# Optimization experiments

Hardware: AMD Instinct MI355X
Metric: run time of the kernel (lower is better)

The kernel has to match this reference:

```python
import jax, jax.numpy as jnp
import numpy as np
from jax.scipy.linalg import solve_triangular

JITTER = 1e-5
BIG = 1e9


def _rq(d2, outscale, ls, alpha):
    # Rational-quadratic kernel (gpytorch RQKernel with outputscale)
    return outscale * (1.0 + d2 / (2.0 * alpha * ls * ls)) ** (-alpha)


def _per_var(tb, m, nz, os_, ls, al, K):
    # tb: [L] times of one sample; m: [L] bool, points belonging to this variable.
    # Sequential GP fantasy updates == prefix conditioning. chol of a leading
    # principal block equals leading block of full chol, so one Cholesky +
    # one triangular solve + cumsum over rows reproduces the sequential loop.
    L = tb.shape[0]
    keyt = jnp.where(m, tb, BIG)
    order = jnp.argsort(keyt)            # this variable's points, time-sorted, first
    ts = tb[order]
    ms = m[order]
    mf = ms.astype(tb.dtype)
    d2 = (ts[:, None] - ts[None, :]) ** 2
    Kxx = _rq(d2, os_, ls, al) * (mf[:, None] * mf[None, :])  # masked rows/cols -> 0
    idx = jnp.arange(L)
    # noisy train covariance; masked points get identity rows (decoupled, zero effect)
    Kn = Kxx.at[idx, idx].set(jnp.where(ms, os_ + nz + JITTER, 1.0))
    C = jnp.linalg.cholesky(Kn)
    v = solve_triangular(C, Kxx, lower=True)     # [L train, L test] (test = same points)
    cum = jnp.cumsum(v * v, axis=0)              # variance explained after i obs
    std_pref = jnp.sqrt(jnp.maximum(os_ - cum, 1e-12)) * mf[None, :]
    sums = std_pref.sum(axis=1)                  # sum of posterior stds after each obs
    s0 = jnp.sqrt(os_) * mf.sum()                # prior sum of stds
    prev = jnp.concatenate([s0[None], sums[:-1]])
    gains = jnp.maximum(prev - sums, 0.0) * mf   # info gain per added observation
    # partition timeline into K groups of near-equal total information
    cg = jnp.cumsum(gains)
    frac = (cg - 0.5 * gains) / jnp.maximum(cg[-1], 1e-12)
    grp = jnp.clip(jnp.floor(frac * K), 0, K - 1).astype(jnp.int32)
    return order, mf, grp, gains


def _forward(t, vid, noise, outputscale, lengthscale, alpha, K):
    B, L = t.shape
    V = noise.shape[0]

    def per_bv(tb, vidb, v):
        m = vidb == v
        order, mf, grp, gains = _per_var(tb, m, noise[v], outputscale[v],
                                         lengthscale[v], alpha[v], K)
        col = v * K + grp
        oh = jnp.zeros((L, V * K), t.dtype).at[order, col].add(mf)
        g = jnp.zeros((L,), t.dtype).at[order].add(gains)
        return oh, g

    def per_b(tb, vidb):
        oh, g = jax.vmap(per_bv, in_axes=(None, None, 0))(tb, vidb, jnp.arange(V))
        return oh.sum(0), g.sum(0)   # variables are disjoint -> sum == union

    return jax.vmap(per_b)(t, vid)


def setup_inputs() -> dict:
    key = jax.random.key(0)
    ks = jax.random.split(key, 7)
    B, L, V = 8, 512, 16
    t = jax.random.uniform(ks[0], (B, L), dtype=jnp.float32)
    y = jax.random.normal(ks[1], (B, L), dtype=jnp.float32)
    vid = jax.random.randint(ks[2], (B, L), 0, V, dtype=jnp.int32)
    noise = 0.01 + 0.05 * jax.random.uniform(ks[3], (V,), dtype=jnp.float32)
    outputscale = 0.5 + jax.random.uniform(ks[4], (V,), dtype=jnp.float32)
    lengthscale = 0.05 + 0.2 * jax.random.uniform(ks[5], (V,), dtype=jnp.float32)
    alpha = 0.5 + jax.random.uniform(ks[6], (V,), dtype=jnp.float32)
    return {"t": t, "y": y, "vid": vid, "noise": noise, "outputscale": outputscale,
            "lengthscale": lengthscale, "alpha": alpha, "hyper_num_nodes": 8}


def reference(t, y, vid, noise, outputscale, lengthscale, alpha, hyper_num_nodes):
    # Returns (mask [B, L, V*K] hard one-hot aggregation mask, gains [B, L] info gain).
    # GP posterior variance does not depend on y, so y only affects training (not here).
    mask, gains = _forward(t, vid, noise, outputscale, lengthscale, alpha, hyper_num_nodes)
    return mask, gains
```

## Files before the change

### kernel.cpp

```cpp
#include <hip/hip_runtime.h>
#include <math.h>

#define NMAX 64
#define JITTER 1e-5


__device__ __forceinline__ double rdlane_f64(double x, int lane) {
    union { double d; int i[2]; } a, r;
    a.d = x;
    r.i[0] = __builtin_amdgcn_readlane(a.i[0], lane);
    r.i[1] = __builtin_amdgcn_readlane(a.i[1], lane);
    return r.d;
}

#define FOR16(M) M(0) M(1) M(2) M(3) M(4) M(5) M(6) M(7) \
                 M(8) M(9) M(10) M(11) M(12) M(13) M(14) M(15)

#define FOR16_J(M, Kc) \
    M(Kc,0)  M(Kc,1)  M(Kc,2)  M(Kc,3)  M(Kc,4)  M(Kc,5)  M(Kc,6)  M(Kc,7) \
    M(Kc,8)  M(Kc,9)  M(Kc,10) M(Kc,11) M(Kc,12) M(Kc,13) M(Kc,14) M(Kc,15)

#define LOADT(j) \
    double c##j = ((w16 + j) == lane) ? cdiag : Klds[lane][w16 + j]; \
    double x##j = ((w16 + j) == lane) ? kdiag : Klds[w16 + j][lane];

#define DECLV(j) double v##j = 0.0;

#define FIN(kc, jc) \
    if constexpr ((jc) > (kc)) { \
        double ljk_ = rdlane_f64(c##kc, w16s + jc); \
        c##jc -= c##kc * ljk_; \
        x##jc -= ljk_ * vvk; \
    }

#define FACT(kc) { \
    double dkk = rdlane_f64(c##kc, w16s + kc);   \
    double inv = rsqrt(dkk); \
    c##kc *= inv;                                \
    double vvk = x##kc * inv;                    \
    v##kc = vvk; \
    FOR16_J(FIN, kc) \
}

#define PUB(j) { panelL[pb][j][lane] = c##j; panelV[pb][j][lane] = v##j; }

#define STD1(j) { \
    cum += v##j * v##j; \
    double var_ = os_ - cum; \
    Klds[w16s + j][lane] = liveC ? sqrt(var_ > 1e-12 ? var_ : 1e-12) : 0.0; \
}

#define HOIST(j) \
    const double ml##j  = panelL[pb][j][lane]; \
    const double mvv##j = panelV[pb][j][lane];

#define TRAILK(kc) { \
    const double lk_ = ml##kc; const double vk_ = mvv##kc; \
    const double2 q0_ = *(const double2*)&panelL[pb][kc][w16s + 0]; \
    const double2 q1_ = *(const double2*)&panelL[pb][kc][w16s + 2]; \
    const double2 q2_ = *(const double2*)&panelL[pb][kc][w16s + 4]; \
    const double2 q3_ = *(const double2*)&panelL[pb][kc][w16s + 6]; \
    const double2 q4_ = *(const double2*)&panelL[pb][kc][w16s + 8]; \
    const double2 q5_ = *(const double2*)&panelL[pb][kc][w16s + 10]; \
    const double2 q6_ = *(const double2*)&panelL[pb][kc][w16s + 12]; \
    const double2 q7_ = *(const double2*)&panelL[pb][kc][w16s + 14]; \
    c0  -= lk_ * q0_.x;  x0  -= q0_.x * vk_; \
    c1  -= lk_ * q0_.y;  x1  -= q0_.y * vk_; \
    c2  -= lk_ * q1_.x;  x2  -= q1_.x * vk_; \
    c3  -= lk_ * q1_.y;  x3  -= q1_.y * vk_; \
    c4  -= lk_ * q2_.x;  x4  -= q2_.x * vk_; \
    c5  -= lk_ * q2_.y;  x5  -= q2_.y * vk_; \
    c6  -= lk_ * q3_.x;  x6  -= q3_.x * vk_; \
    c7  -= lk_ * q3_.y;  x7  -= q3_.y * vk_; \
    c8  -= lk_ * q4_.x;  x8  -= q4_.x * vk_; \
    c9  -= lk_ * q4_.y;  x9  -= q4_.y * vk_; \
    c10 -= lk_ * q5_.x;  x10 -= q5_.x * vk_; \
    c11 -= lk_ * q5_.y;  x11 -= q5_.y * vk_; \
    c12 -= lk_ * q6_.x;  x12 -= q6_.x * vk_; \
    c13 -= lk_ * q6_.y;  x13 -= q6_.y * vk_; \
    c14 -= lk_ * q7_.x;  x14 -= q7_.x * vk_; \
    c15 -= lk_ * q7_.y;  x15 -= q7_.y * vk_; \
}

__global__ __attribute__((amdgpu_flat_work_group_size(256, 256), amdgpu_waves_per_eu(1, 1)))
void gp_mask_kernel(const float* __restrict__ t,
                    const int*   __restrict__ vid,
                    const float* __restrict__ noise,
                    const float* __restrict__ outscale,
                    const float* __restrict__ lscale,
                    const float* __restrict__ alpha,
                    const int*   __restrict__ pK,
                    float* __restrict__ out_mask,
                    float* __restrict__ out_gains,
                    int B, int L, int V)
{
    const int b = blockIdx.x / V;
    const int v = blockIdx.x % V;
    const int tid  = threadIdx.x;
    const int lane = tid & 63;
    const int w16  = (tid >> 6) << 4;
    const int w16s = __builtin_amdgcn_readfirstlane(w16);
    const int ws   = w16s >> 4;
    const int Knodes = pK[0];
    const int VK = V * Knodes;

    __shared__ double Klds[NMAX][NMAX + 1];
    __shared__ double panelL[2][16][NMAX];
    __shared__ double panelV[2][16][NMAX];
    __shared__ double cumL[NMAX];
    __shared__ double psum[4][NMAX];
    __shared__ double ts[NMAX];
    __shared__ float  tu[NMAX];
    __shared__ int    idx_u[NMAX];
    __shared__ int    oidx[NMAX];
    __shared__ int    cnt;

    if ((Knodes & 3) == 0) {
        const int kq = Knodes >> 2;
        const float4 z = make_float4(0.f, 0.f, 0.f, 0.f);
        for (int q = tid; q < L * kq; q += 256) {
            int p = q / kq, g = q - p * kq;
            float4* dst = (float4*)(out_mask + ((size_t)b * L + p) * VK + v * Knodes) + g;
            *dst = z;
        }
    } else {
        for (int q = tid; q < L * Knodes; q += 256) {
            int p = q / Knodes, g = q - p * Knodes;
            out_mask[((size_t)b * L + p) * VK + v * Knodes + g] = 0.0f;
        }
    }

    if (tid == 0) cnt = 0;
    __syncthreads();

    for (int i = tid; i < L; i += 256) {
        if (vid[b * L + i] == v) {
            int p = atomicAdd(&cnt, 1);
            if (p < NMAX) { idx_u[p] = i; tu[p] = t[b * L + i]; }
        }
    }
    __syncthreads();
    int n = __builtin_amdgcn_readfirstlane(cnt);
    if (n > NMAX) n = NMAX;

    if (tid < n) {
        float tv = tu[tid]; int iv = idx_u[tid];
        int r = 0;
        for (int e = 0; e < n; e++) {
            float te = tu[e]; int ie = idx_u[e];
            if (te < tv || (te == tv && ie < iv)) r++;
        }
        ts[r] = (double)tv;
        oidx[r] = iv;
    }
    __syncthreads();

    const double os_ = (double)outscale[v];
    const double nz  = (double)noise[v];
    const double ls  = (double)lscale[v];
    const double al  = (double)alpha[v];
    const double isc = 1.0 / (2.0 * al * ls * ls);
    const double nal = -al;
    const double s_  = nz + JITTER;

    for (int q = tid; q < NMAX * (NMAX + 1); q += 256)
        ((double*)Klds)[q] = 0.0;
    __syncthreads();
    {
        const int P2 = n * (n - 1) / 2;
        for (int e = tid; e < P2; e += 256) {
            int i = (int)((sqrt(8.0 * (double)e + 1.0) + 1.0) * 0.5);
            while (i * (i - 1) / 2 > e) --i;
            while ((i + 1) * i / 2 <= e) ++i;
            int j = e - i * (i - 1) / 2;
            double d = ts[i] - ts[j];
            double u = 1.0 + d * d * isc;
            double val = os_ * exp2(nal * log2(u));
            Klds[i][j] = val;
            Klds[j][i] = val;
        }
    }
    __syncthreads();

    const bool liveC = lane < n;
    const double cdiag = liveC ? (os_ + s_) : 1.0;
    const double kdiag = liveC ? os_ : 0.0;

    FOR16(LOADT)
    FOR16(DECLV)
    __syncthreads();

    const int P = (n + 15) >> 4;
    for (int p = 0; p < P; p++) {
        const int pb = p & 1;
        if (ws == p) {
            FOR16(FACT)
            FOR16(PUB)
        }
        __syncthreads();
        if (ws == p) {
            double cum = (p == 0) ? 0.0 : cumL[lane];
            FOR16(STD1)
            cumL[lane] = cum;
        } else if (ws > p && ws < P) {
            FOR16(HOIST)
            FOR16(TRAILK)
        }
    }
    __syncthreads();

    {
        double ps = 0.0;
        #pragma unroll
        for (int jj = 0; jj < 16; jj++) ps += Klds[lane][w16 + jj];
        psum[ws][lane] = ps;
    }
    __syncthreads();

    if (tid < 64 && n > 0) {
        double s_mine = psum[0][tid] + psum[1][tid] + psum[2][tid] + psum[3][tid];

        double sprev = __shfl(s_mine, (tid == 0) ? 0 : tid - 1, 64);
        double prev  = (tid == 0) ? sqrt(os_) * (double)n : sprev;
        double g = 0.0;
        if (tid < n) {
            g = prev - s_mine;
            if (g < 0.0) g = 0.0;
        }
        double sc = g;
        #pragma unroll
        for (int off = 1; off < 64; off <<= 1) {
            double o = __shfl_up(sc, off, 64);
            if (tid >= off) sc += o;
        }
        double total = __shfl(sc, n - 1, 64);
        if (tid < n) {
            double denom = total > 1e-12 ? total : 1e-12;
            double frac = (sc - 0.5 * g) / denom;
            int grp = (int)floor(frac * (double)Knodes);
            if (grp < 0) grp = 0;
            if (grp > Knodes - 1) grp = Knodes - 1;
            int pnt = oidx[tid];
            out_mask[((size_t)b * L + pnt) * VK + v * Knodes + grp] = 1.0f;
            out_gains[(size_t)b * L + pnt] = (float)g;
        }
    }
}

extern "C" void kernel_launch(void* const* d_in, const int* in_sizes, int n_in,
                              void* d_out, int out_size, void* d_ws, size_t ws_size,
                              hipStream_t stream)
{
    const float* t     = (const float*)d_in[0];
    const int*   vid   = (const int*)d_in[2];
    const float* noise = (const float*)d_in[3];
    const float* osc   = (const float*)d_in[4];
    const float* ls    = (const float*)d_in[5];
    const float* al    = (const float*)d_in[6];
    const int*   pK    = (const int*)d_in[7];

    const int V = in_sizes[3];
    const int L = 512;
    const int B = in_sizes[0] / L;

    float* out_mask  = (float*)d_out;
    float* out_gains = (float*)d_out + ((size_t)out_size - (size_t)B * L);

    gp_mask_kernel<<<B * V, 256, 0, stream>>>(t, vid, noise, osc, ls, al, pK,
                                              out_mask, out_gains, B, L, V);
}
```

Before: 89.20 us.

## Split Cholesky panels into 8-column strips across 8 wavefronts

Changes the blocked Cholesky and solve from four waves owning 16 columns each to eight waves owning 8 columns each, with the block size raised to 512 threads. Panels become narrower, so each factor step has a shorter serial readlane chain, and more waves share the trailing update. In exchange the number of panel iterations and block barriers roughly doubles. The wider block may also lower per-wave register budget and occupancy for the 128 small blocks.

```diff
diff --git a/kernel.cpp b/kernel.cpp
--- a/kernel.cpp
+++ b/kernel.cpp
@@ -13,33 +13,31 @@
     return r.d;
 }
 
-#define FOR16(M) M(0) M(1) M(2) M(3) M(4) M(5) M(6) M(7) \
-                 M(8) M(9) M(10) M(11) M(12) M(13) M(14) M(15)
-
-#define FOR16_J(M, Kc) \
-    M(Kc,0)  M(Kc,1)  M(Kc,2)  M(Kc,3)  M(Kc,4)  M(Kc,5)  M(Kc,6)  M(Kc,7) \
-    M(Kc,8)  M(Kc,9)  M(Kc,10) M(Kc,11) M(Kc,12) M(Kc,13) M(Kc,14) M(Kc,15)
+#define FOR8(M) M(0) M(1) M(2) M(3) M(4) M(5) M(6) M(7)
+
+#define FOR8_J(M, Kc) \
+    M(Kc,0) M(Kc,1) M(Kc,2) M(Kc,3) M(Kc,4) M(Kc,5) M(Kc,6) M(Kc,7)
 
 #define LOADT(j) \
-    double c##j = ((w16 + j) == lane) ? cdiag : Klds[lane][w16 + j]; \
-    double x##j = ((w16 + j) == lane) ? kdiag : Klds[w16 + j][lane];
+    double c##j = ((w8 + j) == lane) ? cdiag : Klds[lane][w8 + j]; \
+    double x##j = ((w8 + j) == lane) ? kdiag : Klds[w8 + j][lane];
 
 #define DECLV(j) double v##j = 0.0;
 
 #define FIN(kc, jc) \
     if constexpr ((jc) > (kc)) { \
-        double ljk_ = rdlane_f64(c##kc, w16s + jc); \
+        double ljk_ = rdlane_f64(c##kc, w8s + jc); \
         c##jc -= c##kc * ljk_; \
         x##jc -= ljk_ * vvk; \
     }
 
 #define FACT(kc) { \
-    double dkk = rdlane_f64(c##kc, w16s + kc);   \
+    double dkk = rdlane_f64(c##kc, w8s + kc);    \
     double inv = rsqrt(dkk); \
     c##kc *= inv;                                \
     double vvk = x##kc * inv;                    \
     v##kc = vvk; \
-    FOR16_J(FIN, kc) \
+    FOR8_J(FIN, kc) \
 }
 
 #define PUB(j) { panelL[pb][j][lane] = c##j; panelV[pb][j][lane] = v##j; }
@@ -47,7 +45,7 @@
 #define STD1(j) { \
     cum += v##j * v##j; \
     double var_ = os_ - cum; \
-    Klds[w16s + j][lane] = liveC ? sqrt(var_ > 1e-12 ? var_ : 1e-12) : 0.0; \
+    Klds[w8s + j][lane] = liveC ? sqrt(var_ > 1e-12 ? var_ : 1e-12) : 0.0; \
 }
 
 #define HOIST(j) \
@@ -56,33 +54,21 @@
 
 #define TRAILK(kc) { \
     const double lk_ = ml##kc; const double vk_ = mvv##kc; \
-    const double2 q0_ = *(const double2*)&panelL[pb][kc][w16s + 0]; \
-    const double2 q1_ = *(const double2*)&panelL[pb][kc][w16s + 2]; \
-    const double2 q2_ = *(const double2*)&panelL[pb][kc][w16s + 4]; \
-    const double2 q3_ = *(const double2*)&panelL[pb][kc][w16s + 6]; \
-    const double2 q4_ = *(const double2*)&panelL[pb][kc][w16s + 8]; \
-    const double2 q5_ = *(const double2*)&panelL[pb][kc][w16s + 10]; \
-    const double2 q6_ = *(const double2*)&panelL[pb][kc][w16s + 12]; \
-    const double2 q7_ = *(const double2*)&panelL[pb][kc][w16s + 14]; \
-    c0  -= lk_ * q0_.x;  x0  -= q0_.x * vk_; \
-    c1  -= lk_ * q0_.y;  x1  -= q0_.y * vk_; \
-    c2  -= lk_ * q1_.x;  x2  -= q1_.x * vk_; \
-    c3  -= lk_ * q1_.y;  x3  -= q1_.y * vk_; \
-    c4  -= lk_ * q2_.x;  x4  -= q2_.x * vk_; \
-    c5  -= lk_ * q2_.y;  x5  -= q2_.y * vk_; \
-    c6  -= lk_ * q3_.x;  x6  -= q3_.x * vk_; \
-    c7  -= lk_ * q3_.y;  x7  -= q3_.y * vk_; \
-    c8  -= lk_ * q4_.x;  x8  -= q4_.x * vk_; \
-    c9  -= lk_ * q4_.y;  x9  -= q4_.y * vk_; \
-    c10 -= lk_ * q5_.x;  x10 -= q5_.x * vk_; \
-    c11 -= lk_ * q5_.y;  x11 -= q5_.y * vk_; \
-    c12 -= lk_ * q6_.x;  x12 -= q6_.x * vk_; \
-    c13 -= lk_ * q6_.y;  x13 -= q6_.y * vk_; \
-    c14 -= lk_ * q7_.x;  x14 -= q7_.x * vk_; \
-    c15 -= lk_ * q7_.y;  x15 -= q7_.y * vk_; \
-}
-
-__global__ __attribute__((amdgpu_flat_work_group_size(256, 256), amdgpu_waves_per_eu(1, 1)))
+    const double2 q0_ = *(const double2*)&panelL[pb][kc][w8s + 0]; \
+    const double2 q1_ = *(const double2*)&panelL[pb][kc][w8s + 2]; \
+    const double2 q2_ = *(const double2*)&panelL[pb][kc][w8s + 4]; \
+    const double2 q3_ = *(const double2*)&panelL[pb][kc][w8s + 6]; \
+    c0 -= lk_ * q0_.x;  x0 -= q0_.x * vk_; \
+    c1 -= lk_ * q0_.y;  x1 -= q0_.y * vk_; \
+    c2 -= lk_ * q1_.x;  x2 -= q1_.x * vk_; \
+    c3 -= lk_ * q1_.y;  x3 -= q1_.y * vk_; \
+    c4 -= lk_ * q2_.x;  x4 -= q2_.x * vk_; \
+    c5 -= lk_ * q2_.y;  x5 -= q2_.y * vk_; \
+    c6 -= lk_ * q3_.x;  x6 -= q3_.x * vk_; \
+    c7 -= lk_ * q3_.y;  x7 -= q3_.y * vk_; \
+}
+
+__global__ __attribute__((amdgpu_flat_work_group_size(512, 512), amdgpu_waves_per_eu(2, 2)))
 void gp_mask_kernel(const float* __restrict__ t,
                     const int*   __restrict__ vid,
                     const float* __restrict__ noise,
@@ -98,17 +84,17 @@
     const int v = blockIdx.x % V;
     const int tid  = threadIdx.x;
     const int lane = tid & 63;
-    const int w16  = (tid >> 6) << 4;
-    const int w16s = __builtin_amdgcn_readfirstlane(w16);
-    const int ws   = w16s >> 4;
+    const int w8   = (tid >> 6) << 3;
+    const int w8s  = __builtin_amdgcn_readfirstlane(w8);
+    const int ws   = w8s >> 3;
     const int Knodes = pK[0];
     const int VK = V * Knodes;
 
     __shared__ double Klds[NMAX][NMAX + 1];
-    __shared__ double panelL[2][16][NMAX];
-    __shared__ double panelV[2][16][NMAX];
+    __shared__ double panelL[2][8][NMAX];
+    __shared__ double panelV[2][8][NMAX];
     __shared__ double cumL[NMAX];
-    __shared__ double psum[4][NMAX];
+    __shared__ double psum[8][NMAX];
     __shared__ double ts[NMAX];
     __shared__ float  tu[NMAX];
     __shared__ int    idx_u[NMAX];
@@ -118,13 +104,13 @@
     if ((Knodes & 3) == 0) {
         const int kq = Knodes >> 2;
         const float4 z = make_float4(0.f, 0.f, 0.f, 0.f);
-        for (int q = tid; q < L * kq; q += 256) {
+        for (int q = tid; q < L * kq; q += 512) {
             int p = q / kq, g = q - p * kq;
             float4* dst = (float4*)(out_mask + ((size_t)b * L + p) * VK + v * Knodes) + g;
             *dst = z;
         }
     } else {
-        for (int q = tid; q < L * Knodes; q += 256) {
+        for (int q = tid; q < L * Knodes; q += 512) {
             int p = q / Knodes, g = q - p * Knodes;
             out_mask[((size_t)b * L + p) * VK + v * Knodes + g] = 0.0f;
         }
@@ -133,7 +119,7 @@
     if (tid == 0) cnt = 0;
     __syncthreads();
 
-    for (int i = tid; i < L; i += 256) {
+    for (int i = tid; i < L; i += 512) {
         if (vid[b * L + i] == v) {
             int p = atomicAdd(&cnt, 1);
             if (p < NMAX) { idx_u[p] = i; tu[p] = t[b * L + i]; }
@@ -163,12 +149,12 @@
     const double nal = -al;
     const double s_  = nz + JITTER;
 
-    for (int q = tid; q < NMAX * (NMAX + 1); q += 256)
+    for (int q = tid; q < NMAX * (NMAX + 1); q += 512)
         ((double*)Klds)[q] = 0.0;
     __syncthreads();
     {
         const int P2 = n * (n - 1) / 2;
-        for (int e = tid; e < P2; e += 256) {
+        for (int e = tid; e < P2; e += 512) {
             int i = (int)((sqrt(8.0 * (double)e + 1.0) + 1.0) * 0.5);
             while (i * (i - 1) / 2 > e) --i;
             while ((i + 1) * i / 2 <= e) ++i;
@@ -186,25 +172,25 @@
     const double cdiag = liveC ? (os_ + s_) : 1.0;
     const double kdiag = liveC ? os_ : 0.0;
 
-    FOR16(LOADT)
-    FOR16(DECLV)
-    __syncthreads();
-
-    const int P = (n + 15) >> 4;
+    FOR8(LOADT)
+    FOR8(DECLV)
+    __syncthreads();
+
+    const int P = (n + 7) >> 3;
     for (int p = 0; p < P; p++) {
         const int pb = p & 1;
         if (ws == p) {
-            FOR16(FACT)
-            FOR16(PUB)
+            FOR8(FACT)
+            FOR8(PUB)
         }
         __syncthreads();
         if (ws == p) {
             double cum = (p == 0) ? 0.0 : cumL[lane];
-            FOR16(STD1)
+            FOR8(STD1)
             cumL[lane] = cum;
         } else if (ws > p && ws < P) {
-            FOR16(HOIST)
-            FOR16(TRAILK)
+            FOR8(HOIST)
+            FOR8(TRAILK)
         }
     }
     __syncthreads();
@@ -212,13 +198,14 @@
     {
         double ps = 0.0;
         #pragma unroll
-        for (int jj = 0; jj < 16; jj++) ps += Klds[lane][w16 + jj];
+        for (int jj = 0; jj < 8; jj++) ps += Klds[lane][w8 + jj];
         psum[ws][lane] = ps;
     }
     __syncthreads();
 
     if (tid < 64 && n > 0) {
-        double s_mine = psum[0][tid] + psum[1][tid] + psum[2][tid] + psum[3][tid];
+        double s_mine = psum[0][tid] + psum[1][tid] + psum[2][tid] + psum[3][tid]
+                      + psum[4][tid] + psum[5][tid] + psum[6][tid] + psum[7][tid];
 
         double sprev = __shfl(s_mine, (tid == 0) ? 0 : tid - 1, 64);
         double prev  = (tid == 0) ? sqrt(os_) * (double)n : sprev;
@@ -266,6 +253,6 @@
     float* out_mask  = (float*)d_out;
     float* out_gains = (float*)d_out + ((size_t)out_size - (size_t)B * L);
 
-    gp_mask_kernel<<<B * V, 256, 0, stream>>>(t, vid, noise, osc, ls, al, pK,
+    gp_mask_kernel<<<B * V, 512, 0, stream>>>(t, vid, noise, osc, ls, al, pK,
                                               out_mask, out_gains, B, L, V);
 }
```

New measurement: 84.92 us. 4.8% less time.
